# Kernel optimization log

Hardware: AMD Instinct MI355X
Metric: run time of the kernel (lower is better)

## Reference

```python
import jax, jax.numpy as jnp
import numpy as np

D_MODEL = 1024
NHEAD = 16
D_K = D_MODEL // NHEAD


def setup_inputs() -> dict:
    key = jax.random.key(0)
    ks = jax.random.split(key, 12)
    B, S = 4, 2048
    s = 1.0 / np.sqrt(D_MODEL)
    inp = {
        'query': jax.random.normal(ks[0], (B, S, D_MODEL), jnp.float32),
        'key': jax.random.normal(ks[1], (B, S, D_MODEL), jnp.float32),
        'value': jax.random.normal(ks[2], (B, S, D_MODEL), jnp.float32),
        'Wq': jax.random.uniform(ks[3], (D_MODEL, D_MODEL), jnp.float32, -s, s),
        'bq': jax.random.uniform(ks[4], (D_MODEL,), jnp.float32, -s, s),
        'Wk': jax.random.uniform(ks[5], (D_MODEL, D_MODEL), jnp.float32, -s, s),
        'bk': jax.random.uniform(ks[6], (D_MODEL,), jnp.float32, -s, s),
        'Wv': jax.random.uniform(ks[7], (D_MODEL, D_MODEL), jnp.float32, -s, s),
        'bv': jax.random.uniform(ks[8], (D_MODEL,), jnp.float32, -s, s),
        'Wo': jax.random.uniform(ks[9], (D_MODEL, D_MODEL), jnp.float32, -s, s),
        'bo': jax.random.uniform(ks[10], (D_MODEL,), jnp.float32, -s, s),
    }
    return inp


def _split_heads(x, B):
    # (B, S, d_model) -> (B, H, S, d_k)
    return x.reshape(B, -1, NHEAD, D_K).transpose(0, 2, 1, 3)


def reference(query, key, value, Wq, bq, Wk, bk, Wv, bv, Wo, bo):
    B = query.shape[0]
    scale = np.sqrt(D_K).astype(np.float32)
    # torch Linear: y = x @ W.T + b
    Q = _split_heads(query @ Wq.T + bq, B)   # (B, H, Sq, d_k)
    K = _split_heads(key @ Wk.T + bk, B)     # (B, H, Sk, d_k)
    V = _split_heads(value @ Wv.T + bv, B)   # (B, H, Sk, d_k)
    scores = jnp.einsum('bhqd,bhkd->bhqk', Q, K) / scale
    attn = jax.nn.softmax(scores, axis=-1)   # dropout p=0 -> identity
    out = jnp.einsum('bhqk,bhkd->bhqd', attn, V)
    out = out.transpose(0, 2, 1, 3).reshape(B, -1, D_MODEL)
    return out @ Wo.T + bo
```

## Files before the change

kernel.cpp:

```cpp
#include <hip/hip_runtime.h>
#include <stdint.h>

typedef __attribute__((ext_vector_type(8))) _Float16 half8;
typedef __attribute__((ext_vector_type(2))) __fp16   fp16x2;
typedef __attribute__((ext_vector_type(4))) float    f32x4;
typedef __attribute__((ext_vector_type(4))) unsigned short us4;

__device__ __forceinline__ unsigned short f2h(float f) {
  union { _Float16 h; unsigned short u; } cv; cv.h = (_Float16)f; return cv.u;
}

__device__ __forceinline__ void async_copy16(void* lds, const void* g) {
  __builtin_amdgcn_global_load_lds(
      (__attribute__((address_space(1))) void*)(void*)g,
      (__attribute__((address_space(3))) void*)lds, 16, 0, 0);
}

union U64 { fp16x2 h2[2]; us4 u4; };

__global__ __launch_bounds__(256) void cvt_all(
    const float* __restrict__ q, const float* __restrict__ k, const float* __restrict__ v,
    const float* __restrict__ wq, const float* __restrict__ wk,
    const float* __restrict__ wv, const float* __restrict__ wo,
    unsigned short* __restrict__ oq, unsigned short* __restrict__ ok,
    unsigned short* __restrict__ ov,
    unsigned short* __restrict__ owq, unsigned short* __restrict__ owk,
    unsigned short* __restrict__ owv, unsigned short* __restrict__ owo) {
  int b = blockIdx.x;
  const float* in; unsigned short* out;
  if      (b < 8192)  { in = q;  out = oq;             }
  else if (b < 16384) { in = k;  out = ok;  b -= 8192; }
  else if (b < 24576) { in = v;  out = ov;  b -= 16384; }
  else if (b < 25600) { in = wq; out = owq; b -= 24576; }
  else if (b < 26624) { in = wk; out = owk; b -= 25600; }
  else if (b < 27648) { in = wv; out = owv; b -= 26624; }
  else                { in = wo; out = owo; b -= 27648; }
  const int i = (b * 256 + threadIdx.x) * 4;
  const float4 x = *(const float4*)(in + i);
  us4 o; o.x = f2h(x.x); o.y = f2h(x.y); o.z = f2h(x.z); o.w = f2h(x.w);
  *(us4*)(out + i) = o;
}

__device__ __forceinline__ void gemm128_core(const unsigned short* __restrict__ A,
                                             const unsigned short* __restrict__ Bw,
                                             int m0, int n0,
                                             unsigned short* As, unsigned short* Bs,
                                             f32x4 acc[4][4]) {
  const int tid  = threadIdx.x;
  const int w    = tid >> 6;
  const int l15  = tid & 15;
  const int quad = (tid >> 4) & 3;
  const int w0 = w & 1, w1 = w >> 1;
  const f32x4 zero4 = {0.f, 0.f, 0.f, 0.f};
#pragma unroll
  for (int mt = 0; mt < 4; ++mt)
#pragma unroll
    for (int nt = 0; nt < 4; ++nt) acc[mt][nt] = zero4;

  int srcR[2], srcC[2];
#pragma unroll
  for (int c = 0; c < 2; ++c) {
    const int idx = c * 256 + tid;
    srcR[c] = idx >> 2;
    srcC[c] = (idx & 3) ^ (srcR[c] & 3) ^ ((srcR[c] >> 2) & 3);
  }
  const int cs = quad ^ (l15 & 3) ^ (l15 >> 2);

  for (int k0 = 0; k0 < 1024; k0 += 32) {
    __syncthreads();
#pragma unroll
    for (int c = 0; c < 2; ++c) {
      async_copy16((char*)As + c * 4096 + w * 1024,
                   A  + (m0 + srcR[c]) * 1024 + k0 + srcC[c] * 8);
      async_copy16((char*)Bs + c * 4096 + w * 1024,
                   Bw + (n0 + srcR[c]) * 1024 + k0 + srcC[c] * 8);
    }
    __syncthreads();
    half8 af[4], bf[4];
#pragma unroll
    for (int mt = 0; mt < 4; ++mt)
      af[mt] = *(const half8*)(As + (w1 * 64 + mt * 16 + l15) * 32 + cs * 8);
#pragma unroll
    for (int nt = 0; nt < 4; ++nt)
      bf[nt] = *(const half8*)(Bs + (w0 * 64 + nt * 16 + l15) * 32 + cs * 8);
#pragma unroll
    for (int mt = 0; mt < 4; ++mt)
#pragma unroll
      for (int nt = 0; nt < 4; ++nt)
        acc[mt][nt] = __builtin_amdgcn_mfma_f32_16x16x32_f16(af[mt], bf[nt], acc[mt][nt], 0, 0, 0);
  }
}

__global__ __launch_bounds__(256) void gemm_qkv(
    const unsigned short* __restrict__ Xq, const unsigned short* __restrict__ Xk,
    const unsigned short* __restrict__ Xv,
    const unsigned short* __restrict__ Wq, const unsigned short* __restrict__ Wk,
    const unsigned short* __restrict__ Wv,
    const float* __restrict__ bq, const float* __restrict__ bk, const float* __restrict__ bv,
    unsigned short* __restrict__ Qo, unsigned short* __restrict__ Ko,
    unsigned short* __restrict__ Vo) {
  __shared__ __align__(16) unsigned short As[128 * 32];
  __shared__ __align__(16) unsigned short Bs[128 * 32];
  const int z = blockIdx.z;
  const unsigned short* A = (z == 0) ? Xq : (z == 1) ? Xk : Xv;
  const unsigned short* W = (z == 0) ? Wq : (z == 1) ? Wk : Wv;
  const float* bias = (z == 0) ? bq : (z == 1) ? bk : bv;
  const int m0 = blockIdx.x * 128, n0 = blockIdx.y * 128;
  f32x4 acc[4][4];
  gemm128_core(A, W, m0, n0, As, Bs, acc);

  const int tid = threadIdx.x;
  const int w = tid >> 6, l15 = tid & 15, quad = (tid >> 4) & 3;
  const int w0 = w & 1, w1 = w >> 1;
  const float qscale = (z == 0) ? 0.18033688011112042f : 1.0f;
#pragma unroll
  for (int mt = 0; mt < 4; ++mt) {
    const int mbase = m0 + w1 * 64 + mt * 16 + quad * 4;
    const int bb = mbase >> 11, s = mbase & 2047;
#pragma unroll
    for (int nt = 0; nt < 4; ++nt) {
      const int col = n0 + w0 * 64 + nt * 16 + l15;
      const float badd = bias[col];
      const int h = col >> 6, d = col & 63;
      if (z < 2) {
        unsigned short* dst = (z == 0) ? Qo : Ko;
#pragma unroll
        for (int r = 0; r < 4; ++r)
          dst[((bb * 16 + h) * 2048 + (s + r)) * 64 + d] = f2h((acc[mt][nt][r] + badd) * qscale);
      } else {
        us4 pk;
#pragma unroll
        for (int r = 0; r < 4; ++r) pk[r] = f2h(acc[mt][nt][r] + badd);
        *(us4*)(Vo + ((bb * 16 + h) * 64 + d) * 2048 + s) = pk;
      }
    }
  }
}

#define PKS 72
__global__ __launch_bounds__(256, 3) void attn_kernel(const unsigned short* __restrict__ Q,
                                                      const unsigned short* __restrict__ K,
                                                      const unsigned short* __restrict__ Vt,
                                                      unsigned short* __restrict__ O) {
  __shared__ __align__(16) unsigned short QP[18432];
  __shared__ __align__(16) unsigned short Ks[64 * 64];
  __shared__ __align__(16) unsigned short Vs[64 * 64];
  const int qt = blockIdx.x, bh = blockIdx.y;
  const int tid = threadIdx.x;
  const int w = tid >> 6, l15 = tid & 15, quad = (tid >> 4) & 3;
  const int cq0 = quad ^ (l15 & 7), cq1 = (4 + quad) ^ (l15 & 7);

  const unsigned short* Qg = Q + (bh * 2048 + qt * 256) * 64;
#pragma unroll
  for (int c = 0; c < 8; ++c) {
    const int idx = c * 256 + tid;
    const int r = idx >> 3, cc = (idx & 7) ^ (r & 7);
    async_copy16((char*)QP + c * 4096 + w * 1024, Qg + r * 64 + cc * 8);
  }
  __syncthreads();
  half8 qf[4][2];
#pragma unroll
  for (int s = 0; s < 4; ++s) {
    const int row = w * 64 + s * 16 + l15;
    qf[s][0] = *(const half8*)(QP + row * 64 + cq0 * 8);
    qf[s][1] = *(const half8*)(QP + row * 64 + cq1 * 8);
  }

  int srcR[2], srcC[2];
#pragma unroll
  for (int c = 0; c < 2; ++c) {
    const int idx = c * 256 + tid;
    srcR[c] = idx >> 3;
    srcC[c] = (idx & 7) ^ (srcR[c] & 7);
  }

  const f32x4 zero4 = {0.f, 0.f, 0.f, 0.f};
  f32x4 acc[4][4];
  f32x4 lsum[4];
#pragma unroll
  for (int s = 0; s < 4; ++s) {
    lsum[s] = zero4;
#pragma unroll
    for (int dt = 0; dt < 4; ++dt) acc[s][dt] = zero4;
  }
  half8 ones;
#pragma unroll
  for (int i = 0; i < 8; ++i) ones[i] = (_Float16)1.0f;

  unsigned short* Pw = QP + w * 4608;
  const unsigned short* Kg0 = K + bh * 2048 * 64;
  const unsigned short* Vg0 = Vt + bh * 131072;

  for (int kt = 0; kt < 32; ++kt) {
    __syncthreads();
    const unsigned short* Kg = Kg0 + kt * 4096;
    const unsigned short* Vg = Vg0 + kt * 64;
#pragma unroll
    for (int c = 0; c < 2; ++c) {
      async_copy16((char*)Ks + c * 4096 + w * 1024, Kg + srcR[c] * 64 + srcC[c] * 8);
      async_copy16((char*)Vs + c * 4096 + w * 1024, Vg + srcR[c] * 2048 + srcC[c] * 8);
    }
    __syncthreads();

#pragma unroll
    for (int nt = 0; nt < 4; ++nt) {
      const int rk = nt * 16 + l15;
      half8 ak0 = *(const half8*)(Ks + rk * 64 + cq0 * 8);
      half8 ak1 = *(const half8*)(Ks + rk * 64 + cq1 * 8);
#pragma unroll
      for (int s = 0; s < 4; ++s) {
        f32x4 z = zero4;
        z = __builtin_amdgcn_mfma_f32_16x16x32_f16(ak0, qf[s][0], z, 0, 0, 0);
        z = __builtin_amdgcn_mfma_f32_16x16x32_f16(ak1, qf[s][1], z, 0, 0, 0);
        U64 u;
        u.h2[0] = __builtin_amdgcn_cvt_pkrtz(__builtin_exp2f(z[0]), __builtin_exp2f(z[1]));
        u.h2[1] = __builtin_amdgcn_cvt_pkrtz(__builtin_exp2f(z[2]), __builtin_exp2f(z[3]));
        *(us4*)(Pw + s * 1152 + l15 * PKS + nt * 16 + quad * 4) = u.u4;
      }
    }
#pragma unroll
    for (int h = 0; h < 2; ++h) {
      const int ch = h ? cq1 : cq0;
      half8 bp[4];
#pragma unroll
      for (int s = 0; s < 4; ++s) {
        bp[s] = *(const half8*)(Pw + s * 1152 + l15 * PKS + h * 32 + quad * 8);
        lsum[s] = __builtin_amdgcn_mfma_f32_16x16x32_f16(ones, bp[s], lsum[s], 0, 0, 0);
      }
#pragma unroll
      for (int dt = 0; dt < 4; ++dt) {
        half8 av = *(const half8*)(Vs + (dt * 16 + l15) * 64 + ch * 8);
#pragma unroll
        for (int s = 0; s < 4; ++s)
          acc[s][dt] = __builtin_amdgcn_mfma_f32_16x16x32_f16(av, bp[s], acc[s][dt], 0, 0, 0);
      }
    }
  }

  const int b = bh >> 4, hd = bh & 15;
#pragma unroll
  for (int s = 0; s < 4; ++s) {
    const float rv = 1.0f / lsum[s][0];
    const int sg = qt * 256 + w * 64 + s * 16 + l15;
    unsigned short* Orow = O + (b * 2048 + sg) * 1024 + hd * 64;
#pragma unroll
    for (int dt = 0; dt < 4; ++dt) {
      U64 u;
      u.h2[0] = __builtin_amdgcn_cvt_pkrtz(acc[s][dt][0] * rv, acc[s][dt][1] * rv);
      u.h2[1] = __builtin_amdgcn_cvt_pkrtz(acc[s][dt][2] * rv, acc[s][dt][3] * rv);
      *(us4*)(Orow + dt * 16 + quad * 4) = u.u4;
    }
  }
}

__global__ __launch_bounds__(256) void gemm_out(const unsigned short* __restrict__ A,
                                                const unsigned short* __restrict__ W,
                                                const float* __restrict__ bias,
                                                float* __restrict__ out) {
  __shared__ __align__(16) unsigned short As[128 * 32];
  __shared__ __align__(16) unsigned short Bs[128 * 32];
  const int m0 = blockIdx.x * 128, n0 = blockIdx.y * 128;
  f32x4 acc[4][4];
  gemm128_core(A, W, m0, n0, As, Bs, acc);
  const int tid = threadIdx.x;
  const int w = tid >> 6, l15 = tid & 15, quad = (tid >> 4) & 3;
  const int w0 = w & 1, w1 = w >> 1;
#pragma unroll
  for (int mt = 0; mt < 4; ++mt) {
    const int mbase = m0 + w1 * 64 + mt * 16 + quad * 4;
#pragma unroll
    for (int nt = 0; nt < 4; ++nt) {
      const int col = n0 + w0 * 64 + nt * 16 + l15;
      const float badd = bias[col];
#pragma unroll
      for (int r = 0; r < 4; ++r)
        out[(mbase + r) * 1024 + col] = acc[mt][nt][r] + badd;
    }
  }
}

extern "C" void kernel_launch(void* const* d_in, const int* in_sizes, int n_in,
                              void* d_out, int out_size, void* d_ws, size_t ws_size,
                              hipStream_t stream) {
  const float* query = (const float*)d_in[0];
  const float* key_  = (const float*)d_in[1];
  const float* value = (const float*)d_in[2];
  const float* Wq = (const float*)d_in[3];
  const float* bq = (const float*)d_in[4];
  const float* Wk = (const float*)d_in[5];
  const float* bk = (const float*)d_in[6];
  const float* Wv = (const float*)d_in[7];
  const float* bv = (const float*)d_in[8];
  const float* Wo = (const float*)d_in[9];
  const float* bo = (const float*)d_in[10];

  unsigned short* ws = (unsigned short*)d_ws;
  unsigned short* xq = ws;
  unsigned short* xk = xq + 8388608;
  unsigned short* xv = xk + 8388608;
  unsigned short* wq = xv + 8388608;
  unsigned short* wk = wq + 1048576;
  unsigned short* wv = wk + 1048576;
  unsigned short* wo = wv + 1048576;
  unsigned short* Qw = wo + 1048576;
  unsigned short* Kw = Qw + 8388608;
  unsigned short* Vw = Kw + 8388608;
  unsigned short* Ow = xq;

  cvt_all<<<28672, 256, 0, stream>>>(query, key_, value, Wq, Wk, Wv, Wo,
                                     xq, xk, xv, wq, wk, wv, wo);
  gemm_qkv<<<dim3(64, 8, 3), 256, 0, stream>>>(xq, xk, xv, wq, wk, wv, bq, bk, bv, Qw, Kw, Vw);
  attn_kernel<<<dim3(8, 64), 256, 0, stream>>>(Qw, Kw, Vw, Ow);
  gemm_out<<<dim3(64, 8), 256, 0, stream>>>(Ow, wo, bo, (float*)d_out);
}
```

Before: 362.9 us.

## Double-buffer LDS tiles in GEMM and attention, widen conversion kernel

The shared GEMM core and the attention kernel now use two LDS buffers. The next K-slice (or the next K/V tile) is prefetched with async global-to-LDS copies while MFMAs run on the current buffer, which also drops one barrier per iteration. This is meant to hide global load latency behind compute. In exchange it doubles tile LDS use, and the attention launch bound falls from 3 to 2 blocks, lowering occupancy. Separately, the fp32-to-fp16 conversion kernel now handles 8 elements per thread with 16-byte stores and half as many blocks.

Measured after the change: 363.4 us. About the same (+0.1%).

```diff
diff --git a/kernel.cpp b/kernel.cpp
--- a/kernel.cpp
+++ b/kernel.cpp
@@ -5,6 +5,7 @@
 typedef __attribute__((ext_vector_type(2))) __fp16   fp16x2;
 typedef __attribute__((ext_vector_type(4))) float    f32x4;
 typedef __attribute__((ext_vector_type(4))) unsigned short us4;
+typedef __attribute__((ext_vector_type(8))) unsigned short us8;
 
 __device__ __forceinline__ unsigned short f2h(float f) {
   union { _Float16 h; unsigned short u; } cv; cv.h = (_Float16)f; return cv.u;
@@ -28,17 +29,20 @@
     unsigned short* __restrict__ owv, unsigned short* __restrict__ owo) {
   int b = blockIdx.x;
   const float* in; unsigned short* out;
-  if      (b < 8192)  { in = q;  out = oq;             }
-  else if (b < 16384) { in = k;  out = ok;  b -= 8192; }
-  else if (b < 24576) { in = v;  out = ov;  b -= 16384; }
-  else if (b < 25600) { in = wq; out = owq; b -= 24576; }
-  else if (b < 26624) { in = wk; out = owk; b -= 25600; }
-  else if (b < 27648) { in = wv; out = owv; b -= 26624; }
-  else                { in = wo; out = owo; b -= 27648; }
-  const int i = (b * 256 + threadIdx.x) * 4;
-  const float4 x = *(const float4*)(in + i);
-  us4 o; o.x = f2h(x.x); o.y = f2h(x.y); o.z = f2h(x.z); o.w = f2h(x.w);
-  *(us4*)(out + i) = o;
+  if      (b < 4096)  { in = q;  out = oq;             }
+  else if (b < 8192)  { in = k;  out = ok;  b -= 4096; }
+  else if (b < 12288) { in = v;  out = ov;  b -= 8192; }
+  else if (b < 12800) { in = wq; out = owq; b -= 12288; }
+  else if (b < 13312) { in = wk; out = owk; b -= 12800; }
+  else if (b < 13824) { in = wv; out = owv; b -= 13312; }
+  else                { in = wo; out = owo; b -= 13824; }
+  const int i = (b * 256 + threadIdx.x) * 8;
+  const float4 x0 = *(const float4*)(in + i);
+  const float4 x1 = *(const float4*)(in + i + 4);
+  us8 o;
+  o[0] = f2h(x0.x); o[1] = f2h(x0.y); o[2] = f2h(x0.z); o[3] = f2h(x0.w);
+  o[4] = f2h(x1.x); o[5] = f2h(x1.y); o[6] = f2h(x1.z); o[7] = f2h(x1.w);
+  *(us8*)(out + i) = o;
 }
 
 __device__ __forceinline__ void gemm128_core(const unsigned short* __restrict__ A,
@@ -66,23 +70,34 @@
   }
   const int cs = quad ^ (l15 & 3) ^ (l15 >> 2);
 
+#pragma unroll
+  for (int c = 0; c < 2; ++c) {
+    async_copy16((char*)As + c * 4096 + w * 1024, A  + (m0 + srcR[c]) * 1024 + srcC[c] * 8);
+    async_copy16((char*)Bs + c * 4096 + w * 1024, Bw + (n0 + srcR[c]) * 1024 + srcC[c] * 8);
+  }
+
   for (int k0 = 0; k0 < 1024; k0 += 32) {
+    const int cur = (k0 >> 5) & 1;
     __syncthreads();
-#pragma unroll
-    for (int c = 0; c < 2; ++c) {
-      async_copy16((char*)As + c * 4096 + w * 1024,
-                   A  + (m0 + srcR[c]) * 1024 + k0 + srcC[c] * 8);
-      async_copy16((char*)Bs + c * 4096 + w * 1024,
-                   Bw + (n0 + srcR[c]) * 1024 + k0 + srcC[c] * 8);
-    }
-    __syncthreads();
+    if (k0 < 992) {
+      const int nb = cur ^ 1;
+#pragma unroll
+      for (int c = 0; c < 2; ++c) {
+        async_copy16((char*)As + nb * 8192 + c * 4096 + w * 1024,
+                     A  + (m0 + srcR[c]) * 1024 + (k0 + 32) + srcC[c] * 8);
+        async_copy16((char*)Bs + nb * 8192 + c * 4096 + w * 1024,
+                     Bw + (n0 + srcR[c]) * 1024 + (k0 + 32) + srcC[c] * 8);
+      }
+    }
+    const unsigned short* Ac = As + cur * 4096;
+    const unsigned short* Bc = Bs + cur * 4096;
     half8 af[4], bf[4];
 #pragma unroll
     for (int mt = 0; mt < 4; ++mt)
-      af[mt] = *(const half8*)(As + (w1 * 64 + mt * 16 + l15) * 32 + cs * 8);
+      af[mt] = *(const half8*)(Ac + (w1 * 64 + mt * 16 + l15) * 32 + cs * 8);
 #pragma unroll
     for (int nt = 0; nt < 4; ++nt)
-      bf[nt] = *(const half8*)(Bs + (w0 * 64 + nt * 16 + l15) * 32 + cs * 8);
+      bf[nt] = *(const half8*)(Bc + (w0 * 64 + nt * 16 + l15) * 32 + cs * 8);
 #pragma unroll
     for (int mt = 0; mt < 4; ++mt)
 #pragma unroll
@@ -99,8 +114,8 @@
     const float* __restrict__ bq, const float* __restrict__ bk, const float* __restrict__ bv,
     unsigned short* __restrict__ Qo, unsigned short* __restrict__ Ko,
     unsigned short* __restrict__ Vo) {
-  __shared__ __align__(16) unsigned short As[128 * 32];
-  __shared__ __align__(16) unsigned short Bs[128 * 32];
+  __shared__ __align__(16) unsigned short As[2 * 128 * 32];
+  __shared__ __align__(16) unsigned short Bs[2 * 128 * 32];
   const int z = blockIdx.z;
   const unsigned short* A = (z == 0) ? Xq : (z == 1) ? Xk : Xv;
   const unsigned short* W = (z == 0) ? Wq : (z == 1) ? Wk : Wv;
@@ -138,13 +153,13 @@
 }
 
 #define PKS 72
-__global__ __launch_bounds__(256, 3) void attn_kernel(const unsigned short* __restrict__ Q,
+__global__ __launch_bounds__(256, 2) void attn_kernel(const unsigned short* __restrict__ Q,
                                                       const unsigned short* __restrict__ K,
                                                       const unsigned short* __restrict__ Vt,
                                                       unsigned short* __restrict__ O) {
   __shared__ __align__(16) unsigned short QP[18432];
-  __shared__ __align__(16) unsigned short Ks[64 * 64];
-  __shared__ __align__(16) unsigned short Vs[64 * 64];
+  __shared__ __align__(16) unsigned short Ks[2 * 4096];
+  __shared__ __align__(16) unsigned short Vs[2 * 4096];
   const int qt = blockIdx.x, bh = blockIdx.y;
   const int tid = threadIdx.x;
   const int w = tid >> 6, l15 = tid & 15, quad = (tid >> 4) & 3;
@@ -174,6 +189,14 @@
     srcC[c] = (idx & 7) ^ (srcR[c] & 7);
   }
 
+  const unsigned short* Kg0 = K + bh * 2048 * 64;
+  const unsigned short* Vg0 = Vt + bh * 131072;
+#pragma unroll
+  for (int c = 0; c < 2; ++c) {
+    async_copy16((char*)Ks + c * 4096 + w * 1024, Kg0 + srcR[c] * 64 + srcC[c] * 8);
+    async_copy16((char*)Vs + c * 4096 + w * 1024, Vg0 + srcR[c] * 2048 + srcC[c] * 8);
+  }
+
   const f32x4 zero4 = {0.f, 0.f, 0.f, 0.f};
   f32x4 acc[4][4];
   f32x4 lsum[4];
@@ -188,25 +211,28 @@
   for (int i = 0; i < 8; ++i) ones[i] = (_Float16)1.0f;
 
   unsigned short* Pw = QP + w * 4608;
-  const unsigned short* Kg0 = K + bh * 2048 * 64;
-  const unsigned short* Vg0 = Vt + bh * 131072;
 
   for (int kt = 0; kt < 32; ++kt) {
+    const int cur = kt & 1;
     __syncthreads();
-    const unsigned short* Kg = Kg0 + kt * 4096;
-    const unsigned short* Vg = Vg0 + kt * 64;
-#pragma unroll
-    for (int c = 0; c < 2; ++c) {
-      async_copy16((char*)Ks + c * 4096 + w * 1024, Kg + srcR[c] * 64 + srcC[c] * 8);
-      async_copy16((char*)Vs + c * 4096 + w * 1024, Vg + srcR[c] * 2048 + srcC[c] * 8);
-    }
-    __syncthreads();
+    if (kt < 31) {
+      const int nb = cur ^ 1;
+      const unsigned short* Kg = Kg0 + (kt + 1) * 4096;
+      const unsigned short* Vg = Vg0 + (kt + 1) * 64;
+#pragma unroll
+      for (int c = 0; c < 2; ++c) {
+        async_copy16((char*)Ks + nb * 8192 + c * 4096 + w * 1024, Kg + srcR[c] * 64 + srcC[c] * 8);
+        async_copy16((char*)Vs + nb * 8192 + c * 4096 + w * 1024, Vg + srcR[c] * 2048 + srcC[c] * 8);
+      }
+    }
+    const unsigned short* Kc = Ks + cur * 4096;
+    const unsigned short* Vc = Vs + cur * 4096;
 
 #pragma unroll
     for (int nt = 0; nt < 4; ++nt) {
       const int rk = nt * 16 + l15;
-      half8 ak0 = *(const half8*)(Ks + rk * 64 + cq0 * 8);
-      half8 ak1 = *(const half8*)(Ks + rk * 64 + cq1 * 8);
+      half8 ak0 = *(const half8*)(Kc + rk * 64 + cq0 * 8);
+      half8 ak1 = *(const half8*)(Kc + rk * 64 + cq1 * 8);
 #pragma unroll
       for (int s = 0; s < 4; ++s) {
         f32x4 z = zero4;
@@ -229,7 +255,7 @@
       }
 #pragma unroll
       for (int dt = 0; dt < 4; ++dt) {
-        half8 av = *(const half8*)(Vs + (dt * 16 + l15) * 64 + ch * 8);
+        half8 av = *(const half8*)(Vc + (dt * 16 + l15) * 64 + ch * 8);
 #pragma unroll
         for (int s = 0; s < 4; ++s)
           acc[s][dt] = __builtin_amdgcn_mfma_f32_16x16x32_f16(av, bp[s], acc[s][dt], 0, 0, 0);
@@ -257,8 +283,8 @@
                                                 const unsigned short* __restrict__ W,
                                                 const float* __restrict__ bias,
                                                 float* __restrict__ out) {
-  __shared__ __align__(16) unsigned short As[128 * 32];
-  __shared__ __align__(16) unsigned short Bs[128 * 32];
+  __shared__ __align__(16) unsigned short As[2 * 128 * 32];
+  __shared__ __align__(16) unsigned short Bs[2 * 128 * 32];
   const int m0 = blockIdx.x * 128, n0 = blockIdx.y * 128;
   f32x4 acc[4][4];
   gemm128_core(A, W, m0, n0, As, Bs, acc);
@@ -307,7 +333,7 @@
   unsigned short* Vw = Kw + 8388608;
   unsigned short* Ow = xq;
 
-  cvt_all<<<28672, 256, 0, stream>>>(query, key_, value, Wq, Wk, Wv, Wo,
+  cvt_all<<<14336, 256, 0, stream>>>(query, key_, value, Wq, Wk, Wv, Wo,
                                      xq, xk, xv, wq, wk, wv, wo);
   gemm_qkv<<<dim3(64, 8, 3), 256, 0, stream>>>(xq, xk, xv, wq, wk, wv, bq, bk, bv, Qw, Kw, Vw);
   attn_kernel<<<dim3(8, 64), 256, 0, stream>>>(Qw, Kw, Vw, Ow);
```
